# Performance work log

Measured on AMD Instinct MI355X. Metric: run time of the kernel, lower is better.

## Reference

```python
import jax, jax.numpy as jnp
import numpy as np


def _unfold2d(x, side):
    # x: (B, C, H, W) -> (B, C, out, out, side, side), stride-1 sliding windows
    H = x.shape[2]
    out = H - side + 1
    idx = jnp.arange(out)[:, None] + jnp.arange(side)[None, :]  # (out, side)
    x = x[:, :, idx, :]        # (B, C, out, side, W)
    x = x[:, :, :, :, idx]     # (B, C, out, side, out, side)
    return jnp.transpose(x, (0, 1, 2, 4, 3, 5))  # (B, C, out, out, side, side)


def setup_inputs() -> dict:
    key = jax.random.key(0)
    k1, k2, k3 = jax.random.split(key, 3)
    img, side, num = 128, 5, 25
    out = img - side + 1  # 124
    x = jax.random.normal(k1, (1, 3, img, img), dtype=jnp.float32)
    w = jax.random.normal(k2, (3, out, out, num, side, side), dtype=jnp.float32)
    q = jax.random.normal(k3, (3, out, out, num, side, side), dtype=jnp.float32)
    return {"x": x, "w": w, "q": q}


def reference(x, w, q):
    side = w.shape[-1]
    # patches: (1, 3, out, out, 1, side, side) -- broadcast replaces torch repeat
    p = _unfold2d(x, side)[:, :, :, :, None, :, :]
    y = (jnp.pi + 2.0 * jnp.arctan(10.0 * (p * w - q))) / (2.0 * jnp.pi)
    y = jnp.log(jnp.prod(y + 0.6, axis=6))  # product over last window dim, then log
    y = jnp.sum(y, axis=5)                   # sum over remaining window dim
    return y  # (1, 3, out, out, num)
```

## Files before the change

kernel.cpp:

```cpp
#include <hip/hip_runtime.h>


#define IMG   128
#define OUT   124
#define NUM   25
#define NPATCH (3 * OUT * OUT)
#define NOUT  (NPATCH * NUM)
#define OPB   256

__device__ __forceinline__ float fast_atan(float z) {
    float az  = __builtin_fabsf(z);
    float r   = __builtin_amdgcn_rcpf(az);
    bool  big = az > 1.0f;
    float t   = big ? r : az;
    float s   = t * t;
    float p   =                     -0.01172120f;
    p = __builtin_fmaf(p, s,         0.05265332f);
    p = __builtin_fmaf(p, s,        -0.11643287f);
    p = __builtin_fmaf(p, s,         0.19354346f);
    p = __builtin_fmaf(p, s,        -0.33262347f);
    p = __builtin_fmaf(p, s,         0.99997726f);
    float a = t * p;
    a = big ? (1.57079632679489662f - a) : a;
    return __builtin_copysignf(a, z);
}

__device__ __forceinline__ void copy16_lds(float* l, const float* g) {
    __builtin_amdgcn_global_load_lds(
        (const __attribute__((address_space(1))) unsigned int*)g,
        (__attribute__((address_space(3))) unsigned int*)l,
        16 , 0 , 0 );
}

__global__ __launch_bounds__(OPB) void dendrite_kernel(
    const float* __restrict__ x,
    const float* __restrict__ w,
    const float* __restrict__ q,
    float* __restrict__ out)
{
    __shared__ float w_lds[OPB * NUM];
    __shared__ float q_lds[OPB * NUM];

    const int tid = threadIdx.x;
    const int wvb = tid & ~63;
    const long long o_base = (long long)blockIdx.x * OPB;
    const int nrem = min(OPB, (int)(NOUT - o_base));
    const int lim4 = (nrem * NUM) >> 2;

    const float* wsrc = w + o_base * NUM;
    const float* qsrc = q + o_base * NUM;

    #pragma unroll
    for (int r = 0; r < 7; ++r) {
        const int idx4 = r * OPB + tid;
        if (idx4 < lim4)
            copy16_lds(&w_lds[(r * OPB + wvb) * 4], wsrc + idx4 * 4);
    }
    #pragma unroll
    for (int r = 0; r < 7; ++r) {
        const int idx4 = r * OPB + tid;
        if (idx4 < lim4)
            copy16_lds(&q_lds[(r * OPB + wvb) * 4], qsrc + idx4 * 4);
    }

    const int o  = (int)o_base + tid;
    const int oc = min(o, NOUT - 1);
    int rem = oc / NUM;
    const int j = rem % OUT;  rem /= OUT;
    const int i = rem % OUT;
    const int c = rem / OUT;
    const float* xp = x + ((long long)c * IMG + i) * IMG + j;

    float xv[NUM];
    #pragma unroll
    for (int u = 0; u < 5; ++u) {
        float4 a;
        __builtin_memcpy(&a, xp + u * IMG, sizeof(float4));
        xv[5*u+0] = a.x; xv[5*u+1] = a.y; xv[5*u+2] = a.z; xv[5*u+3] = a.w;
        xv[5*u+4] = xp[u * IMG + 4];
    }

    asm volatile("s_waitcnt vmcnt(0)" ::: "memory");
    __syncthreads();

    if (tid < nrem) {
        const float* wl = &w_lds[tid * NUM];
        const float* ql = &q_lds[tid * NUM];
        float prod0 = 1.0f, prod1 = 1.0f;
        #pragma unroll
        for (int k = 0; k < NUM; ++k) {
            const float z = 10.0f * __builtin_fmaf(xv[k], wl[k], -ql[k]);
            const float a = fast_atan(z);
            const float term = __builtin_fmaf(a, 0.31830988618379067f, 1.1f);
            if (k & 1) prod1 *= term; else prod0 *= term;
        }
        out[o] = __logf(prod0 * prod1);
    }
}

extern "C" void kernel_launch(void* const* d_in, const int* in_sizes, int n_in,
                              void* d_out, int out_size, void* d_ws, size_t ws_size,
                              hipStream_t stream) {
    const float* x = (const float*)d_in[0];
    const float* w = (const float*)d_in[1];
    const float* q = (const float*)d_in[2];
    float* out = (float*)d_out;

    const int grid = (NOUT + OPB - 1) / OPB;
    dendrite_kernel<<<grid, OPB, 0, stream>>>(x, w, q, out);
}
```

Baseline: 242.8 us.

## Make kernel persistent with double-buffered LDS prefetch of w/q tiles

New measurement: 246.6 us. About the same (+1.6%).

```diff
diff --git a/kernel.cpp b/kernel.cpp
--- a/kernel.cpp
+++ b/kernel.cpp
@@ -1,12 +1,15 @@
 #include <hip/hip_runtime.h>
 
 
-#define IMG   128
-#define OUT   124
-#define NUM   25
-#define NPATCH (3 * OUT * OUT)
-#define NOUT  (NPATCH * NUM)
-#define OPB   256
+#define IMG    128
+#define OUT    124
+#define NUM    25
+#define NOUT   (3 * OUT * OUT * NUM)
+#define OPB    256
+#define NTILES ((NOUT + OPB - 1) / OPB)
+#define PBLK   256
+#define TILEF  (OPB * NUM)
+#define WQF    (NOUT * NUM)
 
 __device__ __forceinline__ float fast_atan(float z) {
     float az  = __builtin_fabsf(z);
@@ -25,11 +28,68 @@
     return __builtin_copysignf(a, z);
 }
 
-__device__ __forceinline__ void copy16_lds(float* l, const float* g) {
+__device__ __forceinline__ void copy16_lds(const float* g, float* l) {
     __builtin_amdgcn_global_load_lds(
         (const __attribute__((address_space(1))) unsigned int*)g,
-        (__attribute__((address_space(3))) unsigned int*)l,
-        16 , 0 , 0 );
+        (__attribute__((address_space(3))) unsigned int*)l, 16, 0, 0);
+}
+__device__ __forceinline__ void copy4_lds(const float* g, float* l) {
+    __builtin_amdgcn_global_load_lds(
+        (const __attribute__((address_space(1))) unsigned int*)g,
+        (__attribute__((address_space(3))) unsigned int*)l, 4, 0, 0);
+}
+
+__device__ __forceinline__ void stage_tile(
+        float* wl, float* ql,
+        const float* __restrict__ w, const float* __restrict__ q,
+        int tile, int wave_f, int lane)
+{
+    const int tb = tile * TILEF;
+    #pragma unroll
+    for (int r = 0; r < 6; ++r) {
+        const int f  = wave_f + r * 256;
+        int sf = tb + f + lane * 4;
+        sf = min(sf, WQF - 4);
+        copy16_lds(w + sf, wl + f);
+        copy16_lds(q + sf, ql + f);
+    }
+    const int f  = wave_f + 1536;
+    int sf = tb + f + lane;
+    sf = min(sf, WQF - 1);
+    copy4_lds(w + sf, wl + f);
+    copy4_lds(q + sf, ql + f);
+}
+
+__device__ __forceinline__ void load_x(
+        float (&xv)[NUM], const float* __restrict__ x, int o)
+{
+    const int oc = min(o, NOUT - 1);
+    int rem = oc / NUM;
+    const int j = rem % OUT;  rem /= OUT;
+    const int i = rem % OUT;
+    const int c = rem / OUT;
+    const float* xp = x + (c * IMG + i) * IMG + j;
+    #pragma unroll
+    for (int u = 0; u < 5; ++u) {
+        float4 a;
+        __builtin_memcpy(&a, xp + u * IMG, sizeof(float4));
+        xv[5*u+0] = a.x; xv[5*u+1] = a.y; xv[5*u+2] = a.z; xv[5*u+3] = a.w;
+        xv[5*u+4] = xp[u * IMG + 4];
+    }
+}
+
+__device__ __forceinline__ float compute25(
+        const float* wl, const float* ql, const float (&xv)[NUM])
+{
+    float prod0 = 1.0f, prod1 = 1.0f;
+    #pragma unroll
+    for (int k = 0; k < NUM; ++k) {
+        const float z = 10.0f * __builtin_fmaf(xv[k], wl[k], -ql[k]);
+        const float a = fast_atan(z);
+        const float term = __builtin_fmaf(a, 0.31830988618379067f, 1.1f);
+        if (k & 1) prod1 *= term; else prod0 *= term;
+    }
+    return __logf(prod0 * prod1);
 }
 
 __global__ __launch_bounds__(OPB) void dendrite_kernel(
@@ -38,63 +98,43 @@
     const float* __restrict__ q,
     float* __restrict__ out)
 {
-    __shared__ float w_lds[OPB * NUM];
-    __shared__ float q_lds[OPB * NUM];
+    __shared__ float w_lds[2][TILEF];
+    __shared__ float q_lds[2][TILEF];
 
-    const int tid = threadIdx.x;
-    const int wvb = tid & ~63;
-    const long long o_base = (long long)blockIdx.x * OPB;
-    const int nrem = min(OPB, (int)(NOUT - o_base));
-    const int lim4 = (nrem * NUM) >> 2;
+    const int tid    = threadIdx.x;
+    const int lane   = tid & 63;
+    const int wave_f = (tid >> 6) * 1600;
 
-    const float* wsrc = w + o_base * NUM;
-    const float* qsrc = q + o_base * NUM;
+    auto step = [&](const float* wl, const float* ql, float* wln, float* qln,
+                    float (&xc)[NUM], float (&xn)[NUM], int t) {
+        const int  tnext    = t + PBLK;
+        const bool has_next = (tnext < NTILES);
+        __builtin_amdgcn_s_barrier();
+        if (has_next) {
+            stage_tile(wln, qln, w, q, tnext, wave_f, lane);
+            asm volatile("s_waitcnt vmcnt(14)" ::: "memory");
+        } else {
+            asm volatile("s_waitcnt vmcnt(0)" ::: "memory");
+        }
+        __builtin_amdgcn_s_barrier();
+        const int o = t * OPB + tid;
+        if (has_next) load_x(xn, x, o + PBLK * OPB);
+        if (o < NOUT)
+            out[o] = compute25(&wl[tid * NUM], &ql[tid * NUM], xc);
+    };
 
-    #pragma unroll
-    for (int r = 0; r < 7; ++r) {
-        const int idx4 = r * OPB + tid;
-        if (idx4 < lim4)
-            copy16_lds(&w_lds[(r * OPB + wvb) * 4], wsrc + idx4 * 4);
-    }
-    #pragma unroll
-    for (int r = 0; r < 7; ++r) {
-        const int idx4 = r * OPB + tid;
-        if (idx4 < lim4)
-            copy16_lds(&q_lds[(r * OPB + wvb) * 4], qsrc + idx4 * 4);
-    }
+    int t = blockIdx.x;
+    float xA[NUM], xB[NUM];
+    stage_tile(w_lds[0], q_lds[0], w, q, t, wave_f, lane);
+    load_x(xA, x, t * OPB + tid);
 
-    const int o  = (int)o_base + tid;
-    const int oc = min(o, NOUT - 1);
-    int rem = oc / NUM;
-    const int j = rem % OUT;  rem /= OUT;
-    const int i = rem % OUT;
-    const int c = rem / OUT;
-    const float* xp = x + ((long long)c * IMG + i) * IMG + j;
-
-    float xv[NUM];
-    #pragma unroll
-    for (int u = 0; u < 5; ++u) {
-        float4 a;
-        __builtin_memcpy(&a, xp + u * IMG, sizeof(float4));
-        xv[5*u+0] = a.x; xv[5*u+1] = a.y; xv[5*u+2] = a.z; xv[5*u+3] = a.w;
-        xv[5*u+4] = xp[u * IMG + 4];
-    }
-
-    asm volatile("s_waitcnt vmcnt(0)" ::: "memory");
-    __syncthreads();
-
-    if (tid < nrem) {
-        const float* wl = &w_lds[tid * NUM];
-        const float* ql = &q_lds[tid * NUM];
-        float prod0 = 1.0f, prod1 = 1.0f;
-        #pragma unroll
-        for (int k = 0; k < NUM; ++k) {
-            const float z = 10.0f * __builtin_fmaf(xv[k], wl[k], -ql[k]);
-            const float a = fast_atan(z);
-            const float term = __builtin_fmaf(a, 0.31830988618379067f, 1.1f);
-            if (k & 1) prod1 *= term; else prod0 *= term;
-        }
-        out[o] = __logf(prod0 * prod1);
+    for (;;) {
+        step(w_lds[0], q_lds[0], w_lds[1], q_lds[1], xA, xB, t);
+        t += PBLK;
+        if (t >= NTILES) break;
+        step(w_lds[1], q_lds[1], w_lds[0], q_lds[0], xB, xA, t);
+        t += PBLK;
+        if (t >= NTILES) break;
     }
 }
 
@@ -106,6 +146,5 @@
     const float* q = (const float*)d_in[2];
     float* out = (float*)d_out;
 
-    const int grid = (NOUT + OPB - 1) / OPB;
-    dendrite_kernel<<<grid, OPB, 0, stream>>>(x, w, q, out);
+    dendrite_kernel<<<PBLK, OPB, 0, stream>>>(x, w, q, out);
 }
```
